# Performance work log

Hardware: AMD Instinct MI355X
Metric: run time of the kernel (lower is better)

Reference implementation:

```python
import jax, jax.numpy as jnp
import numpy as np

B, C_IN, T = 4, 256, 8192
LAYERS, STACKS = 24, 4
RES, GATE, SKIP, K = 128, 256, 128, 3
LPS = LAYERS // STACKS  # layers per stack -> dilation = 2**(i % LPS)
SQRT_HALF = 0.7071067811865476


def setup_inputs() -> dict:
    key = jax.random.key(0)
    ks = jax.random.split(key, 14)
    s = 0.08  # small init so the 24-layer stack stays well-scaled
    inp = {
        "x": jax.random.normal(ks[0], (B, C_IN, T), jnp.float32),
        "first_w": jax.random.normal(ks[1], (RES, C_IN), jnp.float32) * s,
        "first_b": jnp.zeros((RES,), jnp.float32),
        "conv_w": jax.random.normal(ks[2], (LAYERS, GATE, RES, K), jnp.float32) * s,
        "conv_b": jnp.zeros((LAYERS, GATE), jnp.float32),
        "out_w": jax.random.normal(ks[3], (LAYERS, RES, GATE // 2), jnp.float32) * s,
        "out_b": jnp.zeros((LAYERS, RES), jnp.float32),
        "skip_w": jax.random.normal(ks[4], (LAYERS, SKIP, GATE // 2), jnp.float32) * s,
        "skip_b": jnp.zeros((LAYERS, SKIP), jnp.float32),
        "last1_w": jax.random.normal(ks[5], (SKIP, SKIP), jnp.float32) * s,
        "last1_b": jnp.zeros((SKIP,), jnp.float32),
        "last2_w": jax.random.normal(ks[6], (C_IN, SKIP), jnp.float32) * s,
        "last2_b": jnp.zeros((C_IN,), jnp.float32),
    }
    return inp


def _conv1x1(w, b, h):
    # h: [B, C, T], w: [O, C]
    return jnp.einsum('oc,bct->bot', w, h) + b[None, :, None]


def _causal_dilated_conv(h, w, b, dilation):
    # left pad == torch symmetric pad (k-1)*d followed by crop to first T (causal)
    pad = (K - 1) * dilation
    hp = jnp.pad(h, ((0, 0), (0, 0), (pad, 0)))
    y = jax.lax.conv_general_dilated(
        hp, w, window_strides=(1,), padding='VALID',
        rhs_dilation=(dilation,), dimension_numbers=('NCH', 'OIH', 'NCH'))
    return y + b[None, :, None]


def reference(x, first_w, first_b, conv_w, conv_b, out_w, out_b,
              skip_w, skip_b, last1_w, last1_b, last2_w, last2_b):
    h = _conv1x1(first_w, first_b, x)  # [B, RES, T]
    skips = jnp.zeros((x.shape[0], SKIP, x.shape[-1]), h.dtype)
    for i in range(LAYERS):
        d = 2 ** (i % LPS)
        y = _causal_dilated_conv(h, conv_w[i], conv_b[i], d)  # [B, GATE, T]
        a, g = jnp.split(y, 2, axis=1)
        z = jnp.tanh(a) * jax.nn.sigmoid(g)  # gated tanh*sigmoid
        skips = skips + _conv1x1(skip_w[i], skip_b[i], z)
        h = (_conv1x1(out_w[i], out_b[i], z) + h) * SQRT_HALF  # residual
    skips = skips * (1.0 / LAYERS) ** 0.5
    out = jax.nn.relu(skips)
    out = jax.nn.relu(_conv1x1(last1_w, last1_b, out))
    out = _conv1x1(last2_w, last2_b, out)  # logits [B, 256, T]
    return out
```

## Files before the change

### kernel.cpp

```cpp
#include <hip/hip_runtime.h>

#define B 4
#define CIN 256
#define T 8192
#define NL 24
#define SH 0.70710678118654752f
#define SKIP_SCALE 0.20412414523193150f

typedef unsigned short u16;
typedef __attribute__((ext_vector_type(4))) float f32x4;
typedef __attribute__((ext_vector_type(8))) short s16x8;
typedef __attribute__((ext_vector_type(4))) short s16x4;

__device__ inline u16 f2bf(float f) {
  unsigned u = __float_as_uint(f);
  return (u16)((u + 0x7fffu + ((u >> 16) & 1u)) >> 16);
}
__device__ inline float bf2f(u16 h) { return __uint_as_float((unsigned)h << 16); }
__device__ inline float gate_fn(float a, float g) {
  float e2 = __expf(-2.f * fabsf(a));
  float th = (1.f - e2) * __builtin_amdgcn_rcpf(1.f + e2);
  float sg = __builtin_amdgcn_rcpf(1.f + __expf(-g));
  return copysignf(th, a) * sg;
}

__global__ void cvt_all(const float* __restrict__ conv_w, const float* __restrict__ skip_w,
                        const float* __restrict__ out_w, const float* __restrict__ first_w,
                        const float* __restrict__ last1_w, const float* __restrict__ last2_w,
                        u16* __restrict__ wcv, u16* __restrict__ wso, u16* __restrict__ wf,
                        u16* __restrict__ w1, u16* __restrict__ w2) {
  int i = blockIdx.x * 256 + threadIdx.x;
  if (i < 2359296) {
    int c = i & 127, o = (i >> 7) & 255, kk = (i >> 15) % 3, l = (i >> 15) / 3;
    wcv[i] = f2bf(conv_w[(((size_t)l * 256 + o) * 128 + c) * 3 + kk]);
    return;
  }
  i -= 2359296;
  if (i < 786432) {
    int c = i & 127, r = (i >> 7) & 255, l = i >> 15;
    float v = (r < 128) ? skip_w[((size_t)l * 128 + r) * 128 + c]
                        : out_w[((size_t)l * 128 + (r - 128)) * 128 + c];
    wso[i] = f2bf(v);
    return;
  }
  i -= 786432;
  if (i < 32768) { wf[i] = f2bf(first_w[i]); return; }
  i -= 32768;
  if (i < 16384) { w1[i] = f2bf(last1_w[i]); return; }
  i -= 16384;
  if (i < 32768) { w2[i] = f2bf(last2_w[i]); return; }
}
__global__ void sumsb_kernel(const float* __restrict__ sb, float* __restrict__ dst) {
  int c = threadIdx.x;
  float s = 0.f;
  for (int l = 0; l < NL; l++) s += sb[l * 128 + c];
  dst[c] = s;
}

__global__ __launch_bounds__(256, 2)
void first_kernel(const float* __restrict__ x, const u16* __restrict__ wf,
                  const float* __restrict__ fb, float* __restrict__ hf) {
  __shared__ u16 xT[64 * 256];
  const int tid = threadIdx.x, wv = tid >> 6, lane = tid & 63, lo = lane & 15, hi = lane >> 4;
  const int t0 = blockIdx.x * 64, b = blockIdx.y;
  #pragma unroll
  for (int it = 0; it < 16; it++) {
    int idx = tid + it * 256;
    int c = idx >> 4, t4 = (idx & 15) << 2;
    f32x4 v = *(const f32x4*)(x + ((size_t)b * CIN + c) * T + t0 + t4);
    #pragma unroll
    for (int i = 0; i < 4; i++) {
      int t = t4 + i;
      *(u16*)((char*)xT + t * 512 + ((c * 2) ^ ((t & 7) << 4))) = f2bf(v[i]);
    }
  }
  __syncthreads();
  f32x4 acc[2][4];
  #pragma unroll
  for (int m = 0; m < 2; m++)
    #pragma unroll
    for (int n = 0; n < 4; n++) acc[m][n] = (f32x4){0.f, 0.f, 0.f, 0.f};
  #pragma unroll
  for (int s = 0; s < 8; s++) {
    s16x8 af[2], bf[4];
    #pragma unroll
    for (int m = 0; m < 2; m++)
      af[m] = *(const s16x8*)(wf + (size_t)(wv * 32 + m * 16 + lo) * CIN + s * 32 + hi * 8);
    #pragma unroll
    for (int n = 0; n < 4; n++) {
      int t = n * 16 + lo;
      bf[n] = *(const s16x8*)((const char*)xT + t * 512 + ((s * 64 + hi * 16) ^ ((t & 7) << 4)));
    }
    #pragma unroll
    for (int m = 0; m < 2; m++)
      #pragma unroll
      for (int n = 0; n < 4; n++)
        acc[m][n] = __builtin_amdgcn_mfma_f32_16x16x32_bf16(af[m], bf[n], acc[m][n], 0, 0, 0);
  }
  #pragma unroll
  for (int m = 0; m < 2; m++) {
    int c0 = wv * 32 + m * 16 + hi * 4;
    f32x4 bv = *(const f32x4*)(fb + c0);
    #pragma unroll
    for (int n = 0; n < 4; n++) {
      int t = n * 16 + lo;
      *(f32x4*)(hf + ((size_t)b * T + t0 + t) * 128 + c0) = acc[m][n] + bv;
    }
  }
}

__global__ __launch_bounds__(512, 2)
void group_kernel(const float* __restrict__ hf_in, float* __restrict__ hf_out,
                  float* __restrict__ skip,
                  const u16* __restrict__ wcv_g, const float* __restrict__ cb_g,
                  const u16* __restrict__ wso_g, const float* __restrict__ ob_g,
                  int first) {
  extern __shared__ char smem[];
  u16* hHI = (u16*)smem;
  u16* hLO = (u16*)(smem + 65536);
  u16* zh  = (u16*)(smem + 131072);
  const int tid = threadIdx.x, wv = tid >> 6, lane = tid & 63, lo = lane & 15, hi = lane >> 4;
  const int tj = blockIdx.x & 63, b = blockIdx.x >> 6, t0 = tj * 128;

  #pragma unroll
  for (int it = 0; it < 16; it++) {
    int p = tid + it * 512;
    int r = p >> 5, cq = p & 31;
    int t = t0 - 128 + r;
    f32x4 v = (f32x4){0.f, 0.f, 0.f, 0.f};
    if (t >= 0) v = *(const f32x4*)(hf_in + ((size_t)b * T + t) * 128 + cq * 4);
    s16x4 phi, plo;
    #pragma unroll
    for (int q = 0; q < 4; q++) {
      u16 hb = f2bf(v[q]);
      phi[q] = (short)hb;
      plo[q] = (short)f2bf(v[q] - bf2f(hb));
    }
    int off = r * 256 + ((cq * 8) ^ ((r & 7) << 4));
    *(s16x4*)((char*)hHI + off) = phi;
    *(s16x4*)((char*)hLO + off) = plo;
  }
  __syncthreads();

  f32x4 sk[2][8];
  #pragma unroll
  for (int m = 0; m < 2; m++)
    #pragma unroll
    for (int n = 0; n < 8; n++) sk[m][n] = (f32x4){0.f, 0.f, 0.f, 0.f};

  #pragma unroll 1
  for (int j = 0; j < 6; j++) {
    const int d = 1 << j;
    const u16* wc = wcv_g + (size_t)j * 3 * 256 * 128;
    const float* cb = cb_g + j * 256;
    const u16* wsl = wso_g + (size_t)j * 256 * 128;
    const float* ob = ob_g + j * 128;
    const int cmin = (j == 5) ? 2 : (j == 4) ? 1 : 0;

    #pragma unroll
    for (int ci = 0; ci < 4; ci++) {
      const int c = 3 - ci;
      if (c < cmin) continue;

      f32x4 acc[2][4];
      #pragma unroll
      for (int m = 0; m < 2; m++)
        #pragma unroll
        for (int n = 0; n < 4; n++) acc[m][n] = (f32x4){0.f, 0.f, 0.f, 0.f};
      const int oa = wv * 16, og = 128 + wv * 16;
      #pragma unroll
      for (int k = 0; k < 3; k++) {
        const int rb = 64 * c - (2 - k) * d + lo;
        #pragma unroll
        for (int s = 0; s < 4; s++) {
          s16x8 af0 = *(const s16x8*)(wc + (size_t)(k * 256 + oa + lo) * 128 + s * 32 + hi * 8);
          s16x8 af1 = *(const s16x8*)(wc + (size_t)(k * 256 + og + lo) * 128 + s * 32 + hi * 8);
          const int cbyte = s * 64 + hi * 16;
          s16x8 bfr[4];
          #pragma unroll
          for (int n = 0; n < 4; n++) {
            int rr = rb + n * 16;
            if (rr < 0) rr = 0;
            bfr[n] = *(const s16x8*)((const char*)hHI + rr * 256 + (cbyte ^ ((rr & 7) << 4)));
          }
          #pragma unroll
          for (int n = 0; n < 4; n++) {
            acc[0][n] = __builtin_amdgcn_mfma_f32_16x16x32_bf16(af0, bfr[n], acc[0][n], 0, 0, 0);
            acc[1][n] = __builtin_amdgcn_mfma_f32_16x16x32_bf16(af1, bfr[n], acc[1][n], 0, 0, 0);
          }
        }
      }
      {
        f32x4 ba = *(const f32x4*)(cb + oa + hi * 4);
        f32x4 bg = *(const f32x4*)(cb + og + hi * 4);
        #pragma unroll
        for (int n = 0; n < 4; n++) {
          int u = n * 16 + lo;
          s16x4 pk;
          #pragma unroll
          for (int q = 0; q < 4; q++)
            pk[q] = (short)f2bf(gate_fn(acc[0][n][q] + ba[q], acc[1][n][q] + bg[q]));
          *(s16x4*)((char*)zh + u * 256 + (((oa + hi * 4) * 2) ^ ((u & 7) << 4))) = pk;
        }
      }
      __syncthreads();

      if (wv < 4) {
        if (c >= 2) {
          const int ro = wv * 32;
          #pragma unroll
          for (int s = 0; s < 4; s++) {
            s16x8 af0 = *(const s16x8*)(wsl + (size_t)(ro + lo) * 128 + s * 32 + hi * 8);
            s16x8 af1 = *(const s16x8*)(wsl + (size_t)(ro + 16 + lo) * 128 + s * 32 + hi * 8);
            const int cbyte = s * 64 + hi * 16;
            s16x8 bfr[4];
            #pragma unroll
            for (int n = 0; n < 4; n++) {
              int u = n * 16 + lo;
              bfr[n] = *(const s16x8*)((const char*)zh + u * 256 + (cbyte ^ ((u & 7) << 4)));
            }
            #pragma unroll
            for (int n = 0; n < 4; n++) {
              sk[0][(c - 2) * 4 + n] = __builtin_amdgcn_mfma_f32_16x16x32_bf16(af0, bfr[n], sk[0][(c - 2) * 4 + n], 0, 0, 0);
              sk[1][(c - 2) * 4 + n] = __builtin_amdgcn_mfma_f32_16x16x32_bf16(af1, bfr[n], sk[1][(c - 2) * 4 + n], 0, 0, 0);
            }
          }
        }
      } else {
        const int ro = (wv - 4) * 32;
        f32x4 a2[2][4];
        #pragma unroll
        for (int m = 0; m < 2; m++)
          #pragma unroll
          for (int n = 0; n < 4; n++) a2[m][n] = (f32x4){0.f, 0.f, 0.f, 0.f};
        #pragma unroll
        for (int s = 0; s < 4; s++) {
          s16x8 af0 = *(const s16x8*)(wsl + (size_t)(128 + ro + lo) * 128 + s * 32 + hi * 8);
          s16x8 af1 = *(const s16x8*)(wsl + (size_t)(128 + ro + 16 + lo) * 128 + s * 32 + hi * 8);
          const int cbyte = s * 64 + hi * 16;
          s16x8 bfr[4];
          #pragma unroll
          for (int n = 0; n < 4; n++) {
            int u = n * 16 + lo;
            bfr[n] = *(const s16x8*)((const char*)zh + u * 256 + (cbyte ^ ((u & 7) << 4)));
          }
          #pragma unroll
          for (int n = 0; n < 4; n++) {
            a2[0][n] = __builtin_amdgcn_mfma_f32_16x16x32_bf16(af0, bfr[n], a2[0][n], 0, 0, 0);
            a2[1][n] = __builtin_amdgcn_mfma_f32_16x16x32_bf16(af1, bfr[n], a2[1][n], 0, 0, 0);
          }
        }
        #pragma unroll
        for (int m = 0; m < 2; m++) {
          int c0 = ro + m * 16 + hi * 4;
          f32x4 ob4 = *(const f32x4*)(ob + c0);
          #pragma unroll
          for (int n = 0; n < 4; n++) {
            int u = n * 16 + lo;
            int r = 64 * c + u;
            int off = r * 256 + ((c0 * 2) ^ ((r & 7) << 4));
            s16x4 vhi = *(const s16x4*)((const char*)hHI + off);
            s16x4 vlo = *(const s16x4*)((const char*)hLO + off);
            f32x4 hold;
            #pragma unroll
            for (int q = 0; q < 4; q++)
              hold[q] = bf2f((u16)vhi[q]) + bf2f((u16)vlo[q]);
            f32x4 hnew = (a2[m][n] + ob4 + hold) * SH;
            if (j == 5) {
              *(f32x4*)(hf_out + ((size_t)b * T + t0 + (r - 128)) * 128 + c0) = hnew;
            } else {
              s16x4 nhi, nlo;
              #pragma unroll
              for (int q = 0; q < 4; q++) {
                u16 hb = f2bf(hnew[q]);
                nhi[q] = (short)hb;
                nlo[q] = (short)f2bf(hnew[q] - bf2f(hb));
              }
              *(s16x4*)((char*)hHI + off) = nhi;
              *(s16x4*)((char*)hLO + off) = nlo;
            }
          }
        }
      }
      __syncthreads();
    }
  }

  if (wv < 4) {
    #pragma unroll
    for (int m = 0; m < 2; m++) {
      int c0 = wv * 32 + m * 16 + hi * 4;
      #pragma unroll
      for (int nn = 0; nn < 8; nn++) {
        int t = t0 + nn * 16 + lo;
        size_t off = ((size_t)b * T + t) * 128 + c0;
        f32x4 r = sk[m][nn];
        if (!first) r += *(const f32x4*)(skip + off);
        *(f32x4*)(skip + off) = r;
      }
    }
  }
}

__global__ __launch_bounds__(512, 4)
void pair_kernel(const float* __restrict__ hf_in, float* __restrict__ hf_out,
                 float* __restrict__ skip,
                 const u16* __restrict__ wc1, const float* __restrict__ cb1,
                 const u16* __restrict__ ws1, const float* __restrict__ ob1,
                 const u16* __restrict__ wc2, const float* __restrict__ cb2,
                 const u16* __restrict__ ws2, const float* __restrict__ ob2,
                 int d1, int d2, int first) {
  extern __shared__ u16 lds[];
  u16* h_s = lds;
  u16* zh  = lds + 160 * 128;
  const int tid = threadIdx.x, wv = tid >> 6, lane = tid & 63, lo = lane & 15, hi = lane >> 4;
  const int tj = blockIdx.x, b = blockIdx.y, t0 = tj * 64;
  const int R0 = 128 + 2 * d1;

  for (int p = tid; p < R0 * 32; p += 512) {
    int j0 = p >> 5, cq = p & 31;
    int t = t0 - 64 - 2 * d1 + j0;
    f32x4 v = (f32x4){0.f, 0.f, 0.f, 0.f};
    if (t >= 0) v = *(const f32x4*)(hf_in + ((size_t)b * T + t) * 128 + cq * 4);
    s16x4 pk;
    #pragma unroll
    for (int j = 0; j < 4; j++) pk[j] = (short)f2bf(v[j]);
    *(s16x4*)((char*)h_s + j0 * 256 + ((cq * 8) ^ (((j0 + 64 - 2 * d1) & 7) << 4))) = pk;
  }
  __syncthreads();

  f32x4 A[2][8];
  const int oa = wv * 16, og = 128 + wv * 16;

  #pragma unroll
  for (int m = 0; m < 2; m++)
    #pragma unroll
    for (int n = 0; n < 8; n++) A[m][n] = (f32x4){0.f, 0.f, 0.f, 0.f};
  #pragma unroll
  for (int k = 0; k < 3; k++) {
    const int st = ((lo + (k + 6) * d1) & 7) << 4;
    const int jb = k * d1;
    #pragma unroll
    for (int s = 0; s < 4; s++) {
      s16x8 af0 = *(const s16x8*)(wc1 + ((size_t)(k * 256 + oa + lo)) * 128 + s * 32 + hi * 8);
      s16x8 af1 = *(const s16x8*)(wc1 + ((size_t)(k * 256 + og + lo)) * 128 + s * 32 + hi * 8);
      const int cb_ = s * 64 + hi * 16;
      #pragma unroll
      for (int h2 = 0; h2 < 2; h2++) {
        s16x8 bf[4];
        #pragma unroll
        for (int nn = 0; nn < 4; nn++) {
          int j0 = (h2 * 4 + nn) * 16 + lo + jb;
          bf[nn] = *(const s16x8*)((const char*)h_s + j0 * 256 + (cb_ ^ st));
        }
        #pragma unroll
        for (int nn = 0; nn < 4; nn++) {
          A[0][h2 * 4 + nn] = __builtin_amdgcn_mfma_f32_16x16x32_bf16(af0, bf[nn], A[0][h2 * 4 + nn], 0, 0, 0);
          A[1][h2 * 4 + nn] = __builtin_amdgcn_mfma_f32_16x16x32_bf16(af1, bf[nn], A[1][h2 * 4 + nn], 0, 0, 0);
        }
      }
    }
  }
  {
    f32x4 ba = *(const f32x4*)(cb1 + oa + hi * 4);
    f32x4 bg = *(const f32x4*)(cb1 + og + hi * 4);
    #pragma unroll
    for (int n = 0; n < 8; n++) {
      int u = n * 16 + lo;
      s16x4 pk;
      #pragma unroll
      for (int j = 0; j < 4; j++)
        pk[j] = (short)f2bf(gate_fn(A[0][n][j] + ba[j], A[1][n][j] + bg[j]));
      *(s16x4*)((char*)zh + u * 256 + (((oa + hi * 4) * 2) ^ ((lo & 7) << 4))) = pk;
    }
  }
  __syncthreads();

  const int ro = wv * 32;
  if (wv < 4) {
    #pragma unroll
    for (int m = 0; m < 2; m++)
      #pragma unroll
      for (int nn = 0; nn < 4; nn++) A[m][nn + 4] = (f32x4){0.f, 0.f, 0.f, 0.f};
    #pragma unroll
    for (int s = 0; s < 4; s++) {
      s16x8 af0 = *(const s16x8*)(ws1 + (size_t)(ro + lo) * 128 + s * 32 + hi * 8);
      s16x8 af1 = *(const s16x8*)(ws1 + (size_t)(ro + 16 + lo) * 128 + s * 32 + hi * 8);
      const int cb_ = s * 64 + hi * 16;
      s16x8 bf[4];
      #pragma unroll
      for (int nn = 0; nn < 4; nn++) {
        int u = (nn + 4) * 16 + lo;
        bf[nn] = *(const s16x8*)((const char*)zh + u * 256 + (cb_ ^ ((lo & 7) << 4)));
      }
      #pragma unroll
      for (int nn = 0; nn < 4; nn++) {
        A[0][nn + 4] = __builtin_amdgcn_mfma_f32_16x16x32_bf16(af0, bf[nn], A[0][nn + 4], 0, 0, 0);
        A[1][nn + 4] = __builtin_amdgcn_mfma_f32_16x16x32_bf16(af1, bf[nn], A[1][nn + 4], 0, 0, 0);
      }
    }
  } else {
    #pragma unroll
    for (int m = 0; m < 2; m++)
      #pragma unroll
      for (int n = 0; n < 8; n++) A[m][n] = (f32x4){0.f, 0.f, 0.f, 0.f};
    #pragma unroll
    for (int s = 0; s < 4; s++) {
      s16x8 af0 = *(const s16x8*)(ws1 + (size_t)(ro + lo) * 128 + s * 32 + hi * 8);
      s16x8 af1 = *(const s16x8*)(ws1 + (size_t)(ro + 16 + lo) * 128 + s * 32 + hi * 8);
      const int cb_ = s * 64 + hi * 16;
      #pragma unroll
      for (int h2 = 0; h2 < 2; h2++) {
        s16x8 bf[4];
        #pragma unroll
        for (int nn = 0; nn < 4; nn++) {
          int u = (h2 * 4 + nn) * 16 + lo;
          bf[nn] = *(const s16x8*)((const char*)zh + u * 256 + (cb_ ^ ((lo & 7) << 4)));
        }
        #pragma unroll
        for (int nn = 0; nn < 4; nn++) {
          A[0][h2 * 4 + nn] = __builtin_amdgcn_mfma_f32_16x16x32_bf16(af0, bf[nn], A[0][h2 * 4 + nn], 0, 0, 0);
          A[1][h2 * 4 + nn] = __builtin_amdgcn_mfma_f32_16x16x32_bf16(af1, bf[nn], A[1][h2 * 4 + nn], 0, 0, 0);
        }
      }
    }
    #pragma unroll
    for (int m = 0; m < 2; m++) {
      int c0 = (wv - 4) * 32 + m * 16 + hi * 4;
      f32x4 ob4 = *(const f32x4*)(ob1 + c0);
      #pragma unroll
      for (int n = 0; n < 8; n++) {
        int u = n * 16 + lo;
        int t_out = t0 - 64 + u;
        f32x4 h0 = (f32x4){0.f, 0.f, 0.f, 0.f};
        if (t_out >= 0) h0 = *(const f32x4*)(hf_in + ((size_t)b * T + t_out) * 128 + c0);
        f32x4 h1 = (A[m][n] + ob4 + h0) * SH;
        if (t_out < 0) h1 = (f32x4){0.f, 0.f, 0.f, 0.f};
        A[m][n] = h1;
        s16x4 pk;
        #pragma unroll
        for (int j = 0; j < 4; j++) pk[j] = (short)f2bf(h1[j]);
        *(s16x4*)((char*)h_s + u * 256 + ((c0 * 2) ^ ((lo & 7) << 4))) = pk;
      }
    }
  }
  __syncthreads();

  #pragma unroll
  for (int m = 0; m < 2; m++)
    #pragma unroll
    for (int n = 0; n < 4; n++) A[m][n] = (f32x4){0.f, 0.f, 0.f, 0.f};
  #pragma unroll
  for (int k = 0; k < 3; k++) {
    const int st = ((lo + (k + 6) * d2) & 7) << 4;
    const int jb2 = 64 - 2 * d2 + k * d2;
    #pragma unroll
    for (int s = 0; s < 4; s++) {
      s16x8 af0 = *(const s16x8*)(wc2 + ((size_t)(k * 256 + oa + lo)) * 128 + s * 32 + hi * 8);
      s16x8 af1 = *(const s16x8*)(wc2 + ((size_t)(k * 256 + og + lo)) * 128 + s * 32 + hi * 8);
      const int cb_ = s * 64 + hi * 16;
      s16x8 bf[4];
      #pragma unroll
      for (int nn = 0; nn < 4; nn++) {
        int j1 = nn * 16 + lo + jb2;
        bf[nn] = *(const s16x8*)((const char*)h_s + j1 * 256 + (cb_ ^ st));
      }
      #pragma unroll
      for (int nn = 0; nn < 4; nn++) {
        A[0][nn] = __builtin_amdgcn_mfma_f32_16x16x32_bf16(af0, bf[nn], A[0][nn], 0, 0, 0);
        A[1][nn] = __builtin_amdgcn_mfma_f32_16x16x32_bf16(af1, bf[nn], A[1][nn], 0, 0, 0);
      }
    }
  }
  {
    f32x4 ba = *(const f32x4*)(cb2 + oa + hi * 4);
    f32x4 bg = *(const f32x4*)(cb2 + og + hi * 4);
    #pragma unroll
    for (int n = 0; n < 4; n++) {
      int u = n * 16 + lo;
      s16x4 pk;
      #pragma unroll
      for (int j = 0; j < 4; j++)
        pk[j] = (short)f2bf(gate_fn(A[0][n][j] + ba[j], A[1][n][j] + bg[j]));
      *(s16x4*)((char*)zh + u * 256 + (((oa + hi * 4) * 2) ^ ((lo & 7) << 4))) = pk;
    }
  }
  __syncthreads();

  if (wv < 4) {
    #pragma unroll
    for (int s = 0; s < 4; s++) {
      s16x8 af0 = *(const s16x8*)(ws2 + (size_t)(ro + lo) * 128 + s * 32 + hi * 8);
      s16x8 af1 = *(const s16x8*)(ws2 + (size_t)(ro + 16 + lo) * 128 + s * 32 + hi * 8);
      const int cb_ = s * 64 + hi * 16;
      s16x8 bf[4];
      #pragma unroll
      for (int nn = 0; nn < 4; nn++) {
        int u = nn * 16 + lo;
        bf[nn] = *(const s16x8*)((const char*)zh + u * 256 + (cb_ ^ ((lo & 7) << 4)));
      }
      #pragma unroll
      for (int nn = 0; nn < 4; nn++) {
        A[0][nn + 4] = __builtin_amdgcn_mfma_f32_16x16x32_bf16(af0, bf[nn], A[0][nn + 4], 0, 0, 0);
        A[1][nn + 4] = __builtin_amdgcn_mfma_f32_16x16x32_bf16(af1, bf[nn], A[1][nn + 4], 0, 0, 0);
      }
    }
    #pragma unroll
    for (int m = 0; m < 2; m++) {
      int c0 = ro + m * 16 + hi * 4;
      #pragma unroll
      for (int n = 0; n < 4; n++) {
        int t = t0 + n * 16 + lo;
        size_t off = ((size_t)b * T + t) * 128 + c0;
        f32x4 r = A[m][n + 4];
        if (!first) r += *(const f32x4*)(skip + off);
        *(f32x4*)(skip + off) = r;
      }
    }
  } else {
    #pragma unroll
    for (int m = 0; m < 2; m++)
      #pragma unroll
      for (int n = 0; n < 4; n++) A[m][n] = (f32x4){0.f, 0.f, 0.f, 0.f};
    #pragma unroll
    for (int s = 0; s < 4; s++) {
      s16x8 af0 = *(const s16x8*)(ws2 + (size_t)(ro + lo) * 128 + s * 32 + hi * 8);
      s16x8 af1 = *(const s16x8*)(ws2 + (size_t)(ro + 16 + lo) * 128 + s * 32 + hi * 8);
      const int cb_ = s * 64 + hi * 16;
      s16x8 bf[4];
      #pragma unroll
      for (int nn = 0; nn < 4; nn++) {
        int u = nn * 16 + lo;
        bf[nn] = *(const s16x8*)((const char*)zh + u * 256 + (cb_ ^ ((lo & 7) << 4)));
      }
      #pragma unroll
      for (int nn = 0; nn < 4; nn++) {
        A[0][nn] = __builtin_amdgcn_mfma_f32_16x16x32_bf16(af0, bf[nn], A[0][nn], 0, 0, 0);
        A[1][nn] = __builtin_amdgcn_mfma_f32_16x16x32_bf16(af1, bf[nn], A[1][nn], 0, 0, 0);
      }
    }
    #pragma unroll
    for (int m = 0; m < 2; m++) {
      int c0 = (wv - 4) * 32 + m * 16 + hi * 4;
      f32x4 ob4 = *(const f32x4*)(ob2 + c0);
      #pragma unroll
      for (int n = 0; n < 4; n++) {
        int t = t0 + n * 16 + lo;
        f32x4 h2v = (A[m][n] + ob4 + A[m][n + 4]) * SH;
        *(f32x4*)(hf_out + ((size_t)b * T + t) * 128 + c0) = h2v;
      }
    }
  }
}

__global__ __launch_bounds__(256, 2)
void head_kernel(const float* __restrict__ skip, const float* __restrict__ sumsb,
                 const u16* __restrict__ w1, const float* __restrict__ b1v,
                 const u16* __restrict__ w2, const float* __restrict__ b2v,
                 float* __restrict__ out) {
  __shared__ u16 sT[64 * 128];
  __shared__ u16 s1T[64 * 128];
  const int tid = threadIdx.x, wv = tid >> 6, lane = tid & 63, lo = lane & 15, hi = lane >> 4;
  const int t0 = blockIdx.x * 64, b = blockIdx.y;

  #pragma unroll
  for (int it = 0; it < 8; it++) {
    int p = tid + it * 256;
    int t = p >> 5, cq = p & 31;
    f32x4 v = *(const f32x4*)(skip + ((size_t)b * T + t0 + t) * 128 + cq * 4);
    f32x4 sb4 = *(const f32x4*)(sumsb + cq * 4);
    s16x4 pk;
    #pragma unroll
    for (int j = 0; j < 4; j++) pk[j] = (short)f2bf(fmaxf((v[j] + sb4[j]) * SKIP_SCALE, 0.f));
    *(s16x4*)((char*)sT + t * 256 + ((cq * 8) ^ ((t & 7) << 4))) = pk;
  }
  __syncthreads();
  {
    f32x4 acc[2][4];
    #pragma unroll
    for (int m = 0; m < 2; m++)
      #pragma unroll
      for (int n = 0; n < 4; n++) acc[m][n] = (f32x4){0.f, 0.f, 0.f, 0.f};
    #pragma unroll
    for (int s = 0; s < 4; s++) {
      s16x8 af0 = *(const s16x8*)(w1 + (size_t)(wv * 32 + lo) * 128 + s * 32 + hi * 8);
      s16x8 af1 = *(const s16x8*)(w1 + (size_t)(wv * 32 + 16 + lo) * 128 + s * 32 + hi * 8);
      #pragma unroll
      for (int n = 0; n < 4; n++) {
        int t = n * 16 + lo;
        s16x8 bf = *(const s16x8*)((const char*)sT + t * 256 + ((s * 64 + hi * 16) ^ ((t & 7) << 4)));
        acc[0][n] = __builtin_amdgcn_mfma_f32_16x16x32_bf16(af0, bf, acc[0][n], 0, 0, 0);
        acc[1][n] = __builtin_amdgcn_mfma_f32_16x16x32_bf16(af1, bf, acc[1][n], 0, 0, 0);
      }
    }
    #pragma unroll
    for (int m = 0; m < 2; m++) {
      int c0 = wv * 32 + m * 16 + hi * 4;
      f32x4 bv = *(const f32x4*)(b1v + c0);
      #pragma unroll
      for (int n = 0; n < 4; n++) {
        int t = n * 16 + lo;
        s16x4 pk;
        #pragma unroll
        for (int j = 0; j < 4; j++) pk[j] = (short)f2bf(fmaxf(acc[m][n][j] + bv[j], 0.f));
        *(s16x4*)((char*)s1T + t * 256 + ((c0 * 2) ^ ((t & 7) << 4))) = pk;
      }
    }
  }
  __syncthreads();
  {
    f32x4 acc[4][4];
    #pragma unroll
    for (int m = 0; m < 4; m++)
      #pragma unroll
      for (int n = 0; n < 4; n++) acc[m][n] = (f32x4){0.f, 0.f, 0.f, 0.f};
    #pragma unroll
    for (int s = 0; s < 4; s++) {
      s16x8 af[4];
      #pragma unroll
      for (int m = 0; m < 4; m++)
        af[m] = *(const s16x8*)(w2 + (size_t)(wv * 64 + m * 16 + lo) * 128 + s * 32 + hi * 8);
      #pragma unroll
      for (int n = 0; n < 4; n++) {
        int t = n * 16 + lo;
        s16x8 bf = *(const s16x8*)((const char*)s1T + t * 256 + ((s * 64 + hi * 16) ^ ((t & 7) << 4)));
        #pragma unroll
        for (int m = 0; m < 4; m++)
          acc[m][n] = __builtin_amdgcn_mfma_f32_16x16x32_bf16(af[m], bf, acc[m][n], 0, 0, 0);
      }
    }
    #pragma unroll
    for (int m = 0; m < 4; m++) {
      int c0 = wv * 64 + m * 16 + hi * 4;
      f32x4 bv = *(const f32x4*)(b2v + c0);
      #pragma unroll
      for (int n = 0; n < 4; n++) {
        int t = t0 + n * 16 + lo;
        f32x4 r = acc[m][n] + bv;
        #pragma unroll
        for (int j = 0; j < 4; j++) out[((size_t)b * CIN + c0 + j) * T + t] = r[j];
      }
    }
  }
}

extern "C" void kernel_launch(void* const* d_in, const int* in_sizes, int n_in,
                              void* d_out, int out_size, void* d_ws, size_t ws_size,
                              hipStream_t stream) {
  const float* x       = (const float*)d_in[0];
  const float* first_w = (const float*)d_in[1];
  const float* first_b = (const float*)d_in[2];
  const float* conv_w  = (const float*)d_in[3];
  const float* conv_b  = (const float*)d_in[4];
  const float* out_w   = (const float*)d_in[5];
  const float* out_b   = (const float*)d_in[6];
  const float* skip_w  = (const float*)d_in[7];
  const float* skip_b  = (const float*)d_in[8];
  const float* last1_w = (const float*)d_in[9];
  const float* last1_b = (const float*)d_in[10];
  const float* last2_w = (const float*)d_in[11];
  const float* last2_b = (const float*)d_in[12];
  float* outp = (float*)d_out;

  u16* wcv = (u16*)d_ws;
  u16* wso = wcv + (size_t)NL * 3 * 256 * 128;
  u16* wfB = wso + (size_t)NL * 256 * 128;
  u16* w1B = wfB + 128 * 256;
  u16* w2B = w1B + 128 * 128;
  float* sumsb = (float*)(w2B + 256 * 128);
  float* skipF = sumsb + 128;
  float* hfA = (float*)d_out;
  float* hfB = hfA + (size_t)B * T * 128;

  cvt_all<<<12608, 256, 0, stream>>>(conv_w, skip_w, out_w, first_w, last1_w, last2_w,
                                     wcv, wso, wfB, w1B, w2B);
  sumsb_kernel<<<1, 128, 0, stream>>>(skip_b, sumsb);

  dim3 g64(T / 64, B);
  first_kernel<<<g64, 256, 0, stream>>>(x, wfB, first_b, hfA);

  (void)hipFuncSetAttribute((const void*)group_kernel,
                            hipFuncAttributeMaxDynamicSharedMemorySize, 147456);
  (void)hipGetLastError();

  group_kernel<<<dim3(256), dim3(512), 147456, stream>>>(
      hfA, hfB, skipF, wcv, conv_b, wso, out_b, 1);
  hipError_t ce = hipGetLastError();

  if (ce == hipSuccess) {
    for (int g = 1; g < 4; g++) {
      const float* hin = (g & 1) ? hfB : hfA;
      float* hout = (g & 1) ? hfA : hfB;
      group_kernel<<<dim3(256), dim3(512), 147456, stream>>>(
          hin, hout, skipF,
          wcv + (size_t)g * 6 * 3 * 256 * 128, conv_b + (size_t)g * 6 * 256,
          wso + (size_t)g * 6 * 256 * 128, out_b + (size_t)g * 6 * 128, 0);
    }
  } else {
    for (int p = 0; p < NL / 2; p++) {
      int l1 = 2 * p, l2 = 2 * p + 1;
      int d1 = 1 << (l1 % 6), d2 = 1 << (l2 % 6);
      const float* hin = (p & 1) ? hfB : hfA;
      float* hout = (p & 1) ? hfA : hfB;
      pair_kernel<<<g64, 512, 73728, stream>>>(
          hin, hout, skipF,
          wcv + (size_t)l1 * 3 * 256 * 128, conv_b + (size_t)l1 * 256,
          wso + (size_t)l1 * 256 * 128, out_b + (size_t)l1 * 128,
          wcv + (size_t)l2 * 3 * 256 * 128, conv_b + (size_t)l2 * 256,
          wso + (size_t)l2 * 256 * 128, out_b + (size_t)l2 * 128,
          d1, d2, p == 0 ? 1 : 0);
    }
  }
  head_kernel<<<g64, 256, 0, stream>>>(skipF, sumsb, w1B, last1_b, w2B, last2_b, outp);
}
```

Before: 865.0 us.

## Shrink fused six-layer group tile to 64 outputs and drop halo hi/lo precision

The fused six-layer group kernel now covers 64 output timesteps per block instead of 128, with a 128-step halo. This doubles the grid and cuts LDS from 144KB to 80KB so more blocks can be resident per CU. Halo rows now keep only the bf16 high part of the residual, and their residual update uses one 16-row MFMA tile per wave. Only the output chunk keeps the split hi/lo representation. The cost is a larger recompute ratio on the halo and slightly lower precision there.

```diff
diff --git a/kernel.cpp b/kernel.cpp
--- a/kernel.cpp
+++ b/kernel.cpp
@@ -109,21 +109,21 @@
   }
 }
 
-__global__ __launch_bounds__(512, 2)
-void group_kernel(const float* __restrict__ hf_in, float* __restrict__ hf_out,
-                  float* __restrict__ skip,
-                  const u16* __restrict__ wcv_g, const float* __restrict__ cb_g,
-                  const u16* __restrict__ wso_g, const float* __restrict__ ob_g,
-                  int first) {
+__global__ __launch_bounds__(512, 4)
+void group6_kernel(const float* __restrict__ hf_in, float* __restrict__ hf_out,
+                   float* __restrict__ skip,
+                   const u16* __restrict__ wcv_g, const float* __restrict__ cb_g,
+                   const u16* __restrict__ wso_g, const float* __restrict__ ob_g,
+                   int first) {
   extern __shared__ char smem[];
   u16* hHI = (u16*)smem;
-  u16* hLO = (u16*)(smem + 65536);
-  u16* zh  = (u16*)(smem + 131072);
+  u16* hLO = (u16*)(smem + 49152);
+  u16* zh  = (u16*)(smem + 65536);
   const int tid = threadIdx.x, wv = tid >> 6, lane = tid & 63, lo = lane & 15, hi = lane >> 4;
-  const int tj = blockIdx.x & 63, b = blockIdx.x >> 6, t0 = tj * 128;
-
-  #pragma unroll
-  for (int it = 0; it < 16; it++) {
+  const int tj = blockIdx.x, b = blockIdx.y, t0 = tj * 64;
+
+  #pragma unroll
+  for (int it = 0; it < 12; it++) {
     int p = tid + it * 512;
     int r = p >> 5, cq = p & 31;
     int t = t0 - 128 + r;
@@ -136,17 +136,17 @@
       phi[q] = (short)hb;
       plo[q] = (short)f2bf(v[q] - bf2f(hb));
     }
-    int off = r * 256 + ((cq * 8) ^ ((r & 7) << 4));
-    *(s16x4*)((char*)hHI + off) = phi;
-    *(s16x4*)((char*)hLO + off) = plo;
+    int key = (cq * 8) ^ ((r & 7) << 4);
+    *(s16x4*)((char*)hHI + r * 256 + key) = phi;
+    if (r >= 128) *(s16x4*)((char*)hLO + (r - 128) * 256 + key) = plo;
   }
   __syncthreads();
 
-  f32x4 sk[2][8];
+  f32x4 sk[2][4];
   #pragma unroll
   for (int m = 0; m < 2; m++)
     #pragma unroll
-    for (int n = 0; n < 8; n++) sk[m][n] = (f32x4){0.f, 0.f, 0.f, 0.f};
+    for (int n = 0; n < 4; n++) sk[m][n] = (f32x4){0.f, 0.f, 0.f, 0.f};
 
   #pragma unroll 1
   for (int j = 0; j < 6; j++) {
@@ -157,9 +157,9 @@
     const float* ob = ob_g + j * 128;
     const int cmin = (j == 5) ? 2 : (j == 4) ? 1 : 0;
 
-    #pragma unroll
-    for (int ci = 0; ci < 4; ci++) {
-      const int c = 3 - ci;
+    #pragma unroll 1
+    for (int ci = 0; ci < 3; ci++) {
+      const int c = 2 - ci;
       if (c < cmin) continue;
 
       f32x4 acc[2][4];
@@ -205,8 +205,8 @@
       }
       __syncthreads();
 
-      if (wv < 4) {
-        if (c >= 2) {
+      if (c == 2) {
+        if (wv < 4) {
           const int ro = wv * 32;
           #pragma unroll
           for (int s = 0; s < 4; s++) {
@@ -221,22 +221,74 @@
             }
             #pragma unroll
             for (int n = 0; n < 4; n++) {
-              sk[0][(c - 2) * 4 + n] = __builtin_amdgcn_mfma_f32_16x16x32_bf16(af0, bfr[n], sk[0][(c - 2) * 4 + n], 0, 0, 0);
-              sk[1][(c - 2) * 4 + n] = __builtin_amdgcn_mfma_f32_16x16x32_bf16(af1, bfr[n], sk[1][(c - 2) * 4 + n], 0, 0, 0);
+              sk[0][n] = __builtin_amdgcn_mfma_f32_16x16x32_bf16(af0, bfr[n], sk[0][n], 0, 0, 0);
+              sk[1][n] = __builtin_amdgcn_mfma_f32_16x16x32_bf16(af1, bfr[n], sk[1][n], 0, 0, 0);
             }
           }
+        } else {
+          const int ro = (wv - 4) * 32;
+          f32x4 a2[2][4];
+          #pragma unroll
+          for (int m = 0; m < 2; m++)
+            #pragma unroll
+            for (int n = 0; n < 4; n++) a2[m][n] = (f32x4){0.f, 0.f, 0.f, 0.f};
+          #pragma unroll
+          for (int s = 0; s < 4; s++) {
+            s16x8 af0 = *(const s16x8*)(wsl + (size_t)(128 + ro + lo) * 128 + s * 32 + hi * 8);
+            s16x8 af1 = *(const s16x8*)(wsl + (size_t)(128 + ro + 16 + lo) * 128 + s * 32 + hi * 8);
+            const int cbyte = s * 64 + hi * 16;
+            s16x8 bfr[4];
+            #pragma unroll
+            for (int n = 0; n < 4; n++) {
+              int u = n * 16 + lo;
+              bfr[n] = *(const s16x8*)((const char*)zh + u * 256 + (cbyte ^ ((u & 7) << 4)));
+            }
+            #pragma unroll
+            for (int n = 0; n < 4; n++) {
+              a2[0][n] = __builtin_amdgcn_mfma_f32_16x16x32_bf16(af0, bfr[n], a2[0][n], 0, 0, 0);
+              a2[1][n] = __builtin_amdgcn_mfma_f32_16x16x32_bf16(af1, bfr[n], a2[1][n], 0, 0, 0);
+            }
+          }
+          #pragma unroll
+          for (int m = 0; m < 2; m++) {
+            int c0 = ro + m * 16 + hi * 4;
+            f32x4 ob4 = *(const f32x4*)(ob + c0);
+            #pragma unroll
+            for (int n = 0; n < 4; n++) {
+              int u = n * 16 + lo;
+              int r = 128 + u;
+              int key = (c0 * 2) ^ ((r & 7) << 4);
+              s16x4 vhi = *(const s16x4*)((const char*)hHI + r * 256 + key);
+              s16x4 vlo = *(const s16x4*)((const char*)hLO + u * 256 + key);
+              f32x4 hold;
+              #pragma unroll
+              for (int q = 0; q < 4; q++)
+                hold[q] = bf2f((u16)vhi[q]) + bf2f((u16)vlo[q]);
+              f32x4 hnew = (a2[m][n] + ob4 + hold) * SH;
+              if (j == 5) {
+                *(f32x4*)(hf_out + ((size_t)b * T + t0 + u) * 128 + c0) = hnew;
+              } else {
+                s16x4 nhi, nlo;
+                #pragma unroll
+                for (int q = 0; q < 4; q++) {
+                  u16 hb = f2bf(hnew[q]);
+                  nhi[q] = (short)hb;
+                  nlo[q] = (short)f2bf(hnew[q] - bf2f(hb));
+                }
+                *(s16x4*)((char*)hHI + r * 256 + key) = nhi;
+                *(s16x4*)((char*)hLO + u * 256 + key) = nlo;
+              }
+            }
+          }
         }
       } else {
-        const int ro = (wv - 4) * 32;
-        f32x4 a2[2][4];
-        #pragma unroll
-        for (int m = 0; m < 2; m++)
-          #pragma unroll
-          for (int n = 0; n < 4; n++) a2[m][n] = (f32x4){0.f, 0.f, 0.f, 0.f};
+        const int ro = wv * 16;
+        f32x4 a1[4];
+        #pragma unroll
+        for (int n = 0; n < 4; n++) a1[n] = (f32x4){0.f, 0.f, 0.f, 0.f};
         #pragma unroll
         for (int s = 0; s < 4; s++) {
           s16x8 af0 = *(const s16x8*)(wsl + (size_t)(128 + ro + lo) * 128 + s * 32 + hi * 8);
-          s16x8 af1 = *(const s16x8*)(wsl + (size_t)(128 + ro + 16 + lo) * 128 + s * 32 + hi * 8);
           const int cbyte = s * 64 + hi * 16;
           s16x8 bfr[4];
           #pragma unroll
@@ -245,40 +297,26 @@
             bfr[n] = *(const s16x8*)((const char*)zh + u * 256 + (cbyte ^ ((u & 7) << 4)));
           }
           #pragma unroll
-          for (int n = 0; n < 4; n++) {
-            a2[0][n] = __builtin_amdgcn_mfma_f32_16x16x32_bf16(af0, bfr[n], a2[0][n], 0, 0, 0);
-            a2[1][n] = __builtin_amdgcn_mfma_f32_16x16x32_bf16(af1, bfr[n], a2[1][n], 0, 0, 0);
-          }
-        }
-        #pragma unroll
-        for (int m = 0; m < 2; m++) {
-          int c0 = ro + m * 16 + hi * 4;
+          for (int n = 0; n < 4; n++)
+            a1[n] = __builtin_amdgcn_mfma_f32_16x16x32_bf16(af0, bfr[n], a1[n], 0, 0, 0);
+        }
+        {
+          int c0 = ro + hi * 4;
           f32x4 ob4 = *(const f32x4*)(ob + c0);
           #pragma unroll
           for (int n = 0; n < 4; n++) {
             int u = n * 16 + lo;
             int r = 64 * c + u;
-            int off = r * 256 + ((c0 * 2) ^ ((r & 7) << 4));
-            s16x4 vhi = *(const s16x4*)((const char*)hHI + off);
-            s16x4 vlo = *(const s16x4*)((const char*)hLO + off);
+            int key = (c0 * 2) ^ ((r & 7) << 4);
+            s16x4 vhi = *(const s16x4*)((const char*)hHI + r * 256 + key);
             f32x4 hold;
             #pragma unroll
-            for (int q = 0; q < 4; q++)
-              hold[q] = bf2f((u16)vhi[q]) + bf2f((u16)vlo[q]);
-            f32x4 hnew = (a2[m][n] + ob4 + hold) * SH;
-            if (j == 5) {
-              *(f32x4*)(hf_out + ((size_t)b * T + t0 + (r - 128)) * 128 + c0) = hnew;
-            } else {
-              s16x4 nhi, nlo;
-              #pragma unroll
-              for (int q = 0; q < 4; q++) {
-                u16 hb = f2bf(hnew[q]);
-                nhi[q] = (short)hb;
-                nlo[q] = (short)f2bf(hnew[q] - bf2f(hb));
-              }
-              *(s16x4*)((char*)hHI + off) = nhi;
-              *(s16x4*)((char*)hLO + off) = nlo;
-            }
+            for (int q = 0; q < 4; q++) hold[q] = bf2f((u16)vhi[q]);
+            f32x4 hnew = (a1[n] + ob4 + hold) * SH;
+            s16x4 nhi;
+            #pragma unroll
+            for (int q = 0; q < 4; q++) nhi[q] = (short)f2bf(hnew[q]);
+            *(s16x4*)((char*)hHI + r * 256 + key) = nhi;
           }
         }
       }
@@ -291,10 +329,10 @@
     for (int m = 0; m < 2; m++) {
       int c0 = wv * 32 + m * 16 + hi * 4;
       #pragma unroll
-      for (int nn = 0; nn < 8; nn++) {
-        int t = t0 + nn * 16 + lo;
+      for (int n = 0; n < 4; n++) {
+        int t = t0 + n * 16 + lo;
         size_t off = ((size_t)b * T + t) * 128 + c0;
-        f32x4 r = sk[m][nn];
+        f32x4 r = sk[m][n];
         if (!first) r += *(const f32x4*)(skip + off);
         *(f32x4*)(skip + off) = r;
       }
@@ -679,19 +717,18 @@
   dim3 g64(T / 64, B);
   first_kernel<<<g64, 256, 0, stream>>>(x, wfB, first_b, hfA);
 
-  (void)hipFuncSetAttribute((const void*)group_kernel,
-                            hipFuncAttributeMaxDynamicSharedMemorySize, 147456);
+  (void)hipFuncSetAttribute((const void*)group6_kernel,
+                            hipFuncAttributeMaxDynamicSharedMemorySize, 81920);
   (void)hipGetLastError();
 
-  group_kernel<<<dim3(256), dim3(512), 147456, stream>>>(
-      hfA, hfB, skipF, wcv, conv_b, wso, out_b, 1);
+  group6_kernel<<<g64, 512, 81920, stream>>>(hfA, hfB, skipF, wcv, conv_b, wso, out_b, 1);
   hipError_t ce = hipGetLastError();
 
   if (ce == hipSuccess) {
     for (int g = 1; g < 4; g++) {
       const float* hin = (g & 1) ? hfB : hfA;
       float* hout = (g & 1) ? hfA : hfB;
-      group_kernel<<<dim3(256), dim3(512), 147456, stream>>>(
+      group6_kernel<<<g64, 512, 81920, stream>>>(
           hin, hout, skipF,
           wcv + (size_t)g * 6 * 3 * 256 * 128, conv_b + (size_t)g * 6 * 256,
           wso + (size_t)g * 6 * 256 * 128, out_b + (size_t)g * 6 * 128, 0);
```

After: 1.215 ms. 1.4x slower.
